# Kernel tuning notes

Measured on AMD Instinct MI355X. Metric: run time of the kernel, lower is better.

Reference implementation:

```python
import jax, jax.numpy as jnp
import numpy as np

H = 1024   # HIDDEN_DIM
V = 15000  # VOCAB_SIZE
L = 2      # NUM_LAYERS
E = 4      # experts per block
B, S = 32, 2048


def rmsnorm(x, w, eps=1e-6):
    return x * jax.lax.rsqrt(jnp.mean(x * x, axis=-1, keepdims=True) + eps) * w


def setup_inputs() -> dict:
    key = jax.random.key(0)
    ks = jax.random.split(key, 8)
    windows = jax.random.randint(ks[0], (B, S), 0, V, dtype=jnp.int32)
    hemis = jax.random.randint(ks[1], (B,), 0, 2, dtype=jnp.int32)
    experts = jax.random.randint(ks[2], (B,), 0, E, dtype=jnp.int32)
    emb = jax.random.normal(ks[3], (V, H), dtype=jnp.float32) * 0.02
    norm1_w = jnp.ones((L, H), dtype=jnp.float32)
    decay_logit = jnp.full((L, H), 2.0, dtype=jnp.float32)  # torch init: ones*2.0
    norm2_w = jnp.ones((L, H), dtype=jnp.float32)
    # expert weights, torch Linear layout [out, in] per expert: [L, E, H, H]
    Wexp = jax.random.normal(ks[4], (L, E, H, H), dtype=jnp.float32) * 0.02
    final_norm_w = jnp.ones((H,), dtype=jnp.float32)
    lm_head = jax.random.normal(ks[5], (V, H), dtype=jnp.float32) * 0.02
    return dict(windows=windows, hemis=hemis, experts=experts, emb=emb,
                norm1_w=norm1_w, decay_logit=decay_logit, norm2_w=norm2_w,
                Wexp=Wexp, final_norm_w=final_norm_w, lm_head=lm_head)


def reference(windows, hemis, experts, emb, norm1_w, decay_logit, norm2_w,
              Wexp, final_norm_w, lm_head):
    del hemis  # only used for router loss when targets are given (inference path)
    x = emb[windows]  # [B,S,H]
    onehot = jax.nn.one_hot(experts, E, dtype=x.dtype)  # [B,E]
    for l in range(L):
        xn = rmsnorm(x, norm1_w[l])
        decay = jax.nn.sigmoid(decay_logit[l])  # [H]

        def step(state, xt):
            s = state * decay + xt * (1.0 - decay)
            return s, s

        init = jnp.zeros((x.shape[0], H), dtype=x.dtype)
        _, states = jax.lax.scan(step, init, jnp.swapaxes(xn, 0, 1))  # [S,B,H]
        x = x + jnp.swapaxes(states, 0, 1)
        pool = rmsnorm(x, norm2_w[l])[:, -1, :]  # [B,H]
        # all 4 expert FFNs on the pooled state, then select by expert id
        out_all = jax.nn.relu(jnp.einsum('bh,edh->ebd', pool, Wexp[l]))  # [E,B,H]
        out = jnp.einsum('be,ebh->bh', onehot, out_all)  # [B,H]
        x = x + out[:, None, :]
    final_state = rmsnorm(x[:, -1, :], final_norm_w)
    logits = final_state @ lm_head.T  # [B,V]
    return logits
```

## Files before the change

kernel.cpp:

```cpp
#include <hip/hip_runtime.h>
#include <cstddef>

#define H 1024
#define V 15000
#define NE 4
#define B 32
#define S 2048
#define EPS 1e-6f
#define CH 16
#define T0 128

__device__ __forceinline__ float wave_sum(float x) {
#pragma unroll
  for (int off = 32; off > 0; off >>= 1) x += __shfl_down(x, off);
  return x;
}

__global__ __launch_bounds__(256) void k_vocab(const float* __restrict__ emb,
                                               float* __restrict__ invr1) {
  const int gw = (blockIdx.x * blockDim.x + threadIdx.x) >> 6;
  const int lane = threadIdx.x & 63;
  if (gw >= V) return;
  const float4* row = (const float4*)(emb + (size_t)gw * H);
  float s = 0.f;
#pragma unroll
  for (int j = 0; j < 4; ++j) {
    const float4 f = row[lane + 64 * j];
    s += f.x * f.x + f.y * f.y + f.z * f.z + f.w * f.w;
  }
  s = wave_sum(s);
  if (lane == 0) invr1[gw] = rsqrtf(s * (1.f / H) + EPS);
}

__global__ __launch_bounds__(1024, 8) void k_scanA(
    const int* __restrict__ windows, const float* __restrict__ emb,
    const float* __restrict__ norm1_w, const float* __restrict__ decay_logit,
    const float* __restrict__ invr1, float* __restrict__ local1) {
  __shared__ int tok_l[T0];
  __shared__ float iv_l[T0];
  const int b = blockIdx.x / CH, c = blockIdx.x % CH;
  const int h = threadIdx.x;
  if (h < T0) {
    const int tok = windows[b * S + c * T0 + h];
    tok_l[h] = tok << 10;
    iv_l[h] = invr1[tok];
  }
  const float d1 = 1.f / (1.f + expf(-decay_logit[h]));
  const float gw = norm1_w[h] * (1.f - d1);
  __syncthreads();
  float s = 0.f;
  for (int t0 = 0; t0 < T0; t0 += 8) {
    float e[8], cv[8];
#pragma unroll
    for (int k = 0; k < 8; ++k) {
      e[k] = emb[(size_t)tok_l[t0 + k] + h];
      cv[k] = iv_l[t0 + k] * gw;
    }
#pragma unroll
    for (int k = 0; k < 8; ++k) s = s * d1 + e[k] * cv[k];
  }
  local1[(size_t)(b * CH + c) * H + h] = s;
}

__global__ __launch_bounds__(1024) void k_scanB(
    const int* __restrict__ windows, const float* __restrict__ emb,
    const float* __restrict__ decay_logit, const float* __restrict__ local1,
    float* __restrict__ s1start, float* __restrict__ es1,
    float* __restrict__ invp) {
  __shared__ float red[16];
  const int b = blockIdx.x, h = threadIdx.x;
  const float d1 = 1.f / (1.f + expf(-decay_logit[h]));
  float dT = d1;
#pragma unroll
  for (int i = 0; i < 7; ++i) dT *= dT;
  float Sv = 0.f;
  for (int c = 0; c < CH; ++c) {
    const size_t idx = (size_t)(b * CH + c) * H + h;
    s1start[idx] = Sv;
    Sv = dT * Sv + local1[idx];
  }
  const int tl = windows[b * S + S - 1];
  const float v = emb[(size_t)tl * H + h] + Sv;
  es1[b * H + h] = v;
  const float q = wave_sum(v * v);
  if ((h & 63) == 0) red[h >> 6] = q;
  __syncthreads();
  if (h == 0) {
    float t = 0.f;
#pragma unroll
    for (int i = 0; i < 16; ++i) t += red[i];
    invp[b] = rsqrtf(t * (1.f / H) + EPS);
  }
}

__global__ __launch_bounds__(256) void k_expert(const float* __restrict__ src,
    const float* __restrict__ invp, const float* __restrict__ n2w,
    const float* __restrict__ Wl, const int* __restrict__ experts,
    float* __restrict__ outp) {
  __shared__ float p[H];
  const int b = blockIdx.x >> 4;
  const int dblk = blockIdx.x & 15;
  const int tid = threadIdx.x;
  const float ip = invp[b];
  for (int j = tid; j < H; j += 256) p[j] = src[b * H + j] * ip * n2w[j];
  __syncthreads();
  const float* W = Wl + (size_t)experts[b] * H * H;
  const int wave = tid >> 6, lane = tid & 63;
#pragma unroll 1
  for (int i = 0; i < 16; ++i) {
    const int dd = dblk * 64 + wave * 16 + i;
    const float* wr = W + (size_t)dd * H;
    float s = 0.f;
#pragma unroll
    for (int j = 0; j < 16; ++j) s += wr[lane + 64 * j] * p[lane + 64 * j];
    s = wave_sum(s);
    if (lane == 0) outp[b * H + dd] = fmaxf(s, 0.f);
  }
}

__global__ __launch_bounds__(1024, 8) void k_sumsqC(
    const int* __restrict__ windows, const float* __restrict__ emb,
    const float* __restrict__ norm1_w, const float* __restrict__ decay_logit,
    const float* __restrict__ invr1, const float* __restrict__ s1start,
    const float* __restrict__ out1, float* __restrict__ r2) {
  __shared__ int tok_l[T0];
  __shared__ float iv_l[T0];
  __shared__ float q[16 * H];
  const int b = blockIdx.x / CH, c = blockIdx.x % CH;
  const int h = threadIdx.x;
  if (h < T0) {
    const int tok = windows[b * S + c * T0 + h];
    tok_l[h] = tok << 10;
    iv_l[h] = invr1[tok];
  }
  const float d1 = 1.f / (1.f + expf(-decay_logit[h]));
  const float gw = norm1_w[h] * (1.f - d1);
  const float o1 = out1[b * H + h];
  float s1 = s1start[(size_t)(b * CH + c) * H + h];
  __syncthreads();
  const int wv = h >> 6, lane = h & 63;
  for (int sb = 0; sb < T0 / 16; ++sb) {
#pragma unroll
    for (int g = 0; g < 2; ++g) {
      float e[8], cv[8];
#pragma unroll
      for (int k = 0; k < 8; ++k) {
        const int t = sb * 16 + g * 8 + k;
        e[k] = emb[(size_t)tok_l[t] + h];
        cv[k] = iv_l[t] * gw;
      }
#pragma unroll
      for (int k = 0; k < 8; ++k) {
        s1 = s1 * d1 + e[k] * cv[k];
        const float x1 = e[k] + s1 + o1;
        q[(g * 8 + k) * H + h] = x1 * x1;
      }
    }
    __syncthreads();
    const float4* q4 = (const float4*)(q + wv * H);
    float ssum = 0.f;
#pragma unroll
    for (int j = 0; j < 4; ++j) {
      const float4 f = q4[lane + 64 * j];
      ssum += f.x + f.y + f.z + f.w;
    }
    ssum = wave_sum(ssum);
    if (lane == 0) r2[b * S + c * T0 + sb * 16 + wv] = ssum;
    __syncthreads();
  }
}

__global__ __launch_bounds__(256) void k_r2fin(float* __restrict__ r2) {
  const int i = blockIdx.x * 256 + threadIdx.x;
  r2[i] = rsqrtf(r2[i] * (1.f / H) + EPS);
}

__global__ __launch_bounds__(1024, 8) void k_scanD(
    const int* __restrict__ windows, const float* __restrict__ emb,
    const float* __restrict__ norm1_w, const float* __restrict__ decay_logit,
    const float* __restrict__ invr1, const float* __restrict__ s1start,
    const float* __restrict__ out1, const float* __restrict__ r2inv,
    float* __restrict__ local2, float* __restrict__ x1last) {
  __shared__ int tok_l[T0];
  __shared__ float iv_l[T0];
  __shared__ float rv_l[T0];
  const int b = blockIdx.x / CH, c = blockIdx.x % CH;
  const int h = threadIdx.x;
  if (h < T0) {
    const int tok = windows[b * S + c * T0 + h];
    tok_l[h] = tok << 10;
    iv_l[h] = invr1[tok];
    rv_l[h] = r2inv[b * S + c * T0 + h];
  }
  const float d1 = 1.f / (1.f + expf(-decay_logit[h]));
  const float g1 = norm1_w[h] * (1.f - d1);
  const float d2 = 1.f / (1.f + expf(-decay_logit[H + h]));
  const float g2 = norm1_w[H + h] * (1.f - d2);
  const float o1 = out1[b * H + h];
  float s1 = s1start[(size_t)(b * CH + c) * H + h];
  __syncthreads();
  float s2 = 0.f, x1 = 0.f;
  for (int t0 = 0; t0 < T0; t0 += 8) {
    float e[8], cv[8], rc[8];
#pragma unroll
    for (int k = 0; k < 8; ++k) {
      e[k] = emb[(size_t)tok_l[t0 + k] + h];
      cv[k] = iv_l[t0 + k] * g1;
      rc[k] = rv_l[t0 + k] * g2;
    }
#pragma unroll
    for (int k = 0; k < 8; ++k) {
      s1 = s1 * d1 + e[k] * cv[k];
      x1 = e[k] + s1 + o1;
      s2 = s2 * d2 + x1 * rc[k];
    }
  }
  local2[(size_t)(b * CH + c) * H + h] = s2;
  if (c == CH - 1) x1last[b * H + h] = x1;
}

__global__ __launch_bounds__(1024) void k_scanE(
    const float* __restrict__ decay_logit, const float* __restrict__ local2,
    const float* __restrict__ x1last, float* __restrict__ es2,
    float* __restrict__ invp) {
  __shared__ float red[16];
  const int b = blockIdx.x, h = threadIdx.x;
  const float d2 = 1.f / (1.f + expf(-decay_logit[H + h]));
  float dT = d2;
#pragma unroll
  for (int i = 0; i < 7; ++i) dT *= dT;
  float Sv = 0.f;
  for (int c = 0; c < CH; ++c)
    Sv = dT * Sv + local2[(size_t)(b * CH + c) * H + h];
  const float v = x1last[b * H + h] + Sv;
  es2[b * H + h] = v;
  const float q = wave_sum(v * v);
  if ((h & 63) == 0) red[h >> 6] = q;
  __syncthreads();
  if (h == 0) {
    float t = 0.f;
#pragma unroll
    for (int i = 0; i < 16; ++i) t += red[i];
    invp[32 + b] = rsqrtf(t * (1.f / H) + EPS);
  }
}

__global__ __launch_bounds__(256) void k_fstate(const float* __restrict__ es2,
    const float* __restrict__ out2, const float* __restrict__ fnw,
    float* __restrict__ fst) {
  __shared__ float red[4];
  const int b = blockIdx.x, tid = threadIdx.x;
  float4 x = ((const float4*)(es2 + b * H))[tid];
  const float4 y = ((const float4*)(out2 + b * H))[tid];
  x.x += y.x; x.y += y.y; x.z += y.z; x.w += y.w;
  float s = x.x * x.x + x.y * x.y + x.z * x.z + x.w * x.w;
  s = wave_sum(s);
  if ((tid & 63) == 0) red[tid >> 6] = s;
  __syncthreads();
  const float ir =
      rsqrtf((red[0] + red[1] + red[2] + red[3]) * (1.f / H) + EPS);
  const float4 w = ((const float4*)fnw)[tid];
  float4 o;
  o.x = x.x * ir * w.x; o.y = x.y * ir * w.y;
  o.z = x.z * ir * w.z; o.w = x.w * ir * w.w;
  ((float4*)(fst + b * H))[tid] = o;
}

__global__ __launch_bounds__(256) void k_logits(const float* __restrict__ fst,
    const float* __restrict__ lm, float* __restrict__ outp) {
  __shared__ float4 fs4[16 * 256];
  const int bgrp = blockIdx.x & 1;
  const int vblk = blockIdx.x >> 1;
  const int tid = threadIdx.x;
  const float4* src4 = (const float4*)(fst + bgrp * 16 * H);
  for (int j = tid; j < 16 * 256; j += 256) fs4[j] = src4[j];
  __syncthreads();
  const int wave = tid >> 6, lane = tid & 63;
  const int sg = lane >> 4;
  const int c = lane & 15;
  const int u = vblk * 4 + wave;
  if (u >= (V + 15) / 16) return;
  const int v0 = u * 16 + sg * 4;
  const float4* rp[4];
#pragma unroll
  for (int i = 0; i < 4; ++i) {
    int r = v0 + i;
    if (r > V - 1) r = V - 1;
    rp[i] = (const float4*)(lm + (size_t)r * H);
  }
  float acc[4][16];
#pragma unroll
  for (int i = 0; i < 4; ++i)
#pragma unroll
    for (int bb = 0; bb < 16; ++bb) acc[i][bb] = 0.f;
#pragma unroll 4
  for (int jj = 0; jj < 16; ++jj) {
    const int hoff = c + 16 * jj;
    float4 lv[4];
#pragma unroll
    for (int i = 0; i < 4; ++i) lv[i] = rp[i][hoff];
#pragma unroll
    for (int bb = 0; bb < 16; ++bb) {
      const float4 fv = fs4[bb * 256 + hoff];
#pragma unroll
      for (int i = 0; i < 4; ++i) {
        acc[i][bb] += lv[i].x * fv.x + lv[i].y * fv.y + lv[i].z * fv.z +
                      lv[i].w * fv.w;
      }
    }
  }
#pragma unroll
  for (int off = 1; off < 16; off <<= 1)
#pragma unroll
    for (int i = 0; i < 4; ++i)
#pragma unroll
      for (int bb = 0; bb < 16; ++bb)
        acc[i][bb] += __shfl_xor(acc[i][bb], off);
  if (c == 0) {
    const int b0 = bgrp * 16;
#pragma unroll
    for (int bb = 0; bb < 16; ++bb)
#pragma unroll
      for (int i = 0; i < 4; ++i) {
        const int r = v0 + i;
        if (r < V) outp[(size_t)(b0 + bb) * V + r] = acc[i][bb];
      }
  }
}

extern "C" void kernel_launch(void* const* d_in, const int* in_sizes, int n_in,
                              void* d_out, int out_size, void* d_ws,
                              size_t ws_size, hipStream_t stream) {
  const int* windows = (const int*)d_in[0];
  const int* experts = (const int*)d_in[2];
  const float* emb = (const float*)d_in[3];
  const float* norm1_w = (const float*)d_in[4];
  const float* decay_logit = (const float*)d_in[5];
  const float* norm2_w = (const float*)d_in[6];
  const float* Wexp = (const float*)d_in[7];
  const float* final_norm_w = (const float*)d_in[8];
  const float* lm_head = (const float*)d_in[9];
  float* outp = (float*)d_out;

  float* ws = (float*)d_ws;
  float* invr1 = ws;
  float* local1 = invr1 + 15360;
  float* s1start = local1 + B * CH * H;
  float* local2 = s1start + B * CH * H;
  float* out1 = local2 + B * CH * H;
  float* out2 = out1 + B * H;
  float* es1 = out2 + B * H;
  float* es2 = es1 + B * H;
  float* x1last = es2 + B * H;
  float* fst = x1last + B * H;
  float* invp = fst + B * H;
  float* r2 = invp + 64;

  k_vocab<<<(V * 64 + 255) / 256, 256, 0, stream>>>(emb, invr1);
  k_scanA<<<B * CH, 1024, 0, stream>>>(windows, emb, norm1_w, decay_logit,
                                       invr1, local1);
  k_scanB<<<B, 1024, 0, stream>>>(windows, emb, decay_logit, local1, s1start,
                                  es1, invp);
  k_expert<<<B * 16, 256, 0, stream>>>(es1, invp, norm2_w, Wexp, experts,
                                       out1);
  k_sumsqC<<<B * CH, 1024, 0, stream>>>(windows, emb, norm1_w, decay_logit,
                                        invr1, s1start, out1, r2);
  k_r2fin<<<(B * S) / 256, 256, 0, stream>>>(r2);
  k_scanD<<<B * CH, 1024, 0, stream>>>(windows, emb, norm1_w, decay_logit,
                                       invr1, s1start, out1, r2, local2,
                                       x1last);
  k_scanE<<<B, 1024, 0, stream>>>(decay_logit, local2, x1last, es2, invp);
  k_expert<<<B * 16, 256, 0, stream>>>(es2, invp + 32, norm2_w + H,
                                       Wexp + (size_t)NE * H * H, experts,
                                       out2);
  k_fstate<<<B, 256, 0, stream>>>(es2, out2, final_norm_w, fst);
  k_logits<<<512, 256, 0, stream>>>(fst, lm_head, outp);
}
```

Measured before the change: 349.6 us.

## Split logits GEMV over hidden halves with partial buffers and combine kernel

The lm_head projection is split across two halves of the hidden dimension, doubling the block count so more CUs participate. Partial results go to a scratch buffer that reuses dead workspace, and a new kernel sums them into the output. The inner loop also register-prefetches the next lm_head chunk. This costs an extra launch and extra partial-buffer traffic.

```diff
diff --git a/kernel.cpp b/kernel.cpp
--- a/kernel.cpp
+++ b/kernel.cpp
@@ -9,6 +9,7 @@
 #define EPS 1e-6f
 #define CH 16
 #define T0 128
+#define NU 938
 
 __device__ __forceinline__ float wave_sum(float x) {
 #pragma unroll
@@ -267,47 +268,56 @@
 }
 
 __global__ __launch_bounds__(256) void k_logits(const float* __restrict__ fst,
-    const float* __restrict__ lm, float* __restrict__ outp) {
-  __shared__ float4 fs4[16 * 256];
-  const int bgrp = blockIdx.x & 1;
-  const int vblk = blockIdx.x >> 1;
+    const float* __restrict__ lm, float* __restrict__ part) {
+  __shared__ float4 fs4[16 * 128];
+  const int hh = blockIdx.x & 1;
+  const int bgrp = (blockIdx.x >> 1) & 1;
+  const int vblk = blockIdx.x >> 2;
   const int tid = threadIdx.x;
-  const float4* src4 = (const float4*)(fst + bgrp * 16 * H);
-  for (int j = tid; j < 16 * 256; j += 256) fs4[j] = src4[j];
+  for (int j = tid; j < 16 * 128; j += 256) {
+    const int bb = j >> 7, q = j & 127;
+    fs4[j] = ((const float4*)fst)[(bgrp * 16 + bb) * 256 + hh * 128 + q];
+  }
   __syncthreads();
   const int wave = tid >> 6, lane = tid & 63;
   const int sg = lane >> 4;
   const int c = lane & 15;
   const int u = vblk * 4 + wave;
-  if (u >= (V + 15) / 16) return;
+  if (u >= NU) return;
   const int v0 = u * 16 + sg * 4;
   const float4* rp[4];
 #pragma unroll
   for (int i = 0; i < 4; ++i) {
     int r = v0 + i;
     if (r > V - 1) r = V - 1;
-    rp[i] = (const float4*)(lm + (size_t)r * H);
+    rp[i] = (const float4*)(lm + (size_t)r * H) + hh * 128;
   }
   float acc[4][16];
 #pragma unroll
   for (int i = 0; i < 4; ++i)
 #pragma unroll
     for (int bb = 0; bb < 16; ++bb) acc[i][bb] = 0.f;
-#pragma unroll 4
-  for (int jj = 0; jj < 16; ++jj) {
+  float4 lv[4], lvn[4];
+#pragma unroll
+  for (int i = 0; i < 4; ++i) lv[i] = rp[i][c];
+#pragma unroll 1
+  for (int jj = 0; jj < 8; ++jj) {
     const int hoff = c + 16 * jj;
-    float4 lv[4];
-#pragma unroll
-    for (int i = 0; i < 4; ++i) lv[i] = rp[i][hoff];
+    if (jj < 7) {
+#pragma unroll
+      for (int i = 0; i < 4; ++i) lvn[i] = rp[i][hoff + 16];
+    }
 #pragma unroll
     for (int bb = 0; bb < 16; ++bb) {
-      const float4 fv = fs4[bb * 256 + hoff];
+      const float4 fv = fs4[bb * 128 + hoff];
 #pragma unroll
       for (int i = 0; i < 4; ++i) {
         acc[i][bb] += lv[i].x * fv.x + lv[i].y * fv.y + lv[i].z * fv.z +
                       lv[i].w * fv.w;
       }
     }
+#pragma unroll
+    for (int i = 0; i < 4; ++i) lv[i] = lvn[i];
   }
 #pragma unroll
   for (int off = 1; off < 16; off <<= 1)
@@ -317,15 +327,21 @@
       for (int bb = 0; bb < 16; ++bb)
         acc[i][bb] += __shfl_xor(acc[i][bb], off);
   if (c == 0) {
-    const int b0 = bgrp * 16;
+    float* pdst = part + (size_t)hh * B * V + (size_t)bgrp * 16 * V;
 #pragma unroll
     for (int bb = 0; bb < 16; ++bb)
 #pragma unroll
       for (int i = 0; i < 4; ++i) {
         const int r = v0 + i;
-        if (r < V) outp[(size_t)(b0 + bb) * V + r] = acc[i][bb];
+        if (r < V) pdst[(size_t)bb * V + r] = acc[i][bb];
       }
   }
+}
+
+__global__ __launch_bounds__(256) void k_comb(const float* __restrict__ part,
+                                              float* __restrict__ outp) {
+  const int i = blockIdx.x * 256 + threadIdx.x;
+  if (i < B * V) outp[i] = part[i] + part[B * V + i];
 }
 
 extern "C" void kernel_launch(void* const* d_in, const int* in_sizes, int n_in,
@@ -355,6 +371,7 @@
   float* fst = x1last + B * H;
   float* invp = fst + B * H;
   float* r2 = invp + 64;
+  float* part = local1;
 
   k_vocab<<<(V * 64 + 255) / 256, 256, 0, stream>>>(emb, invr1);
   k_scanA<<<B * CH, 1024, 0, stream>>>(windows, emb, norm1_w, decay_logit,
@@ -374,5 +391,6 @@
                                        Wexp + (size_t)NE * H * H, experts,
                                        out2);
   k_fstate<<<B, 256, 0, stream>>>(es2, out2, final_norm_w, fst);
-  k_logits<<<512, 256, 0, stream>>>(fst, lm_head, outp);
-}
+  k_logits<<<940, 256, 0, stream>>>(fst, lm_head, part);
+  k_comb<<<(B * V + 255) / 256, 256, 0, stream>>>(part, outp);
+}
```

Result: no change. 354.4 us (+1.4%).
